# Optimization experiments

Hardware: AMD Instinct MI355X
Metric: run time of the kernel (lower is better)

Reference implementation:

```python
import jax, jax.numpy as jnp
import numpy as np

N = 50000    # nodes
R = 3        # relations
E = 600000   # edges per relation
IN, HID, OUT = 128, 64, 64


def setup_inputs() -> dict:
    key = jax.random.key(0)
    k = jax.random.split(key, 5)
    x = jax.random.normal(k[0], (N, IN), dtype=jnp.float32)
    src = jax.random.randint(k[1], (R, E), 0, N, dtype=jnp.int32)
    dst = jax.random.randint(k[2], (R, E), 0, N, dtype=jnp.int32)
    # glorot-ish init like dgl.nn.GraphConv weight; bias init zeros
    W1 = jax.random.normal(k[3], (R, IN, HID), dtype=jnp.float32) * (IN ** -0.5)
    b1 = jnp.zeros((R, HID), dtype=jnp.float32)
    W2 = jax.random.normal(k[4], (R, HID, OUT), dtype=jnp.float32) * (HID ** -0.5)
    b2 = jnp.zeros((R, OUT), dtype=jnp.float32)
    return {"x": x, "W1": W1, "b1": b1, "W2": W2, "b2": b2, "src": src, "dst": dst}


def _graph_conv(x, src, dst, W, b):
    """dgl.nn.GraphConv with norm='both', single relation.
    x: [N, Fin]; src/dst: [E] int; W: [Fin, Fout]; b: [Fout].
    """
    n = x.shape[0]
    ones = jnp.ones(src.shape[0], dtype=x.dtype)
    out_deg = jax.ops.segment_sum(ones, src, num_segments=n)
    h = x * (jnp.maximum(out_deg, 1.0) ** -0.5)[:, None]   # src-side norm
    if W.shape[0] > W.shape[1]:
        # mult W first, then aggregate (fewer flops per edge)
        h = h @ W
        agg = jax.ops.segment_sum(h[src], dst, num_segments=n)  # [N, Fout]
    else:
        agg = jax.ops.segment_sum(h[src], dst, num_segments=n) @ W
    in_deg = jax.ops.segment_sum(ones, dst, num_segments=n)
    return agg * (jnp.maximum(in_deg, 1.0) ** -0.5)[:, None] + b


def _hetero_conv(x, src, dst, W, b):
    # HeteroGraphConv(aggregate='sum'): run each relation's GraphConv, sum results.
    per_rel = jax.vmap(_graph_conv, in_axes=(None, 0, 0, 0, 0))(x, src, dst, W, b)
    return per_rel.sum(axis=0)  # [N, Fout]


def reference(x, W1, b1, W2, b2, src, dst):
    h = jax.nn.relu(_hetero_conv(x, src, dst, W1, b1))
    return _hetero_conv(h, src, dst, W2, b2)
```

## Files before the change

kernel.cpp:

```cpp
#include <hip/hip_runtime.h>

#define NODES 50000
#define RELS  3
#define NEDGE 600000
#define FIN   128
#define FHID  64
#define FOUT  64
#define SEGS  (RELS * NODES)
#define NBLK  ((SEGS + 255) / 256)

#define HC     96
#define HCHUNK (NEDGE / HC)
#define HBYTES NODES
#define HWORDS (HBYTES / 4)

#define BS     250
#define NBUK   200
#define NBUKT  (RELS * NBUK)
#define CAPLOG 12
#define CAP    (1 << CAPLOG)
#define BCH    192
#define BCHUNK (NEDGE / BCH)

typedef _Float16 half8 __attribute__((ext_vector_type(8)));
typedef float   floatx4 __attribute__((ext_vector_type(4)));

__global__ __launch_bounds__(256) void init_kernel(int* __restrict__ bcur,
                                                   const float* __restrict__ W1,
                                                   const float* __restrict__ W2,
                                                   _Float16* __restrict__ W1t,
                                                   _Float16* __restrict__ W2t) {
    int gid = blockIdx.x * 256 + threadIdx.x;
    if (gid < NBUKT) bcur[gid] = 0;
    int g2 = gid - 1024;
    if (g2 >= 0 && g2 < RELS * FIN * FHID) {
        int r = g2 / (FIN * FHID);
        int rem = g2 - r * FIN * FHID;
        int k = rem / FHID, j = rem - k * FHID;
        W1t[((size_t)r * FHID + j) * FIN + k] = (_Float16)W1[g2];
        return;
    }
    int g3 = g2 - RELS * FIN * FHID;
    if (g3 >= 0 && g3 < RELS * FHID * FOUT) {
        int r = g3 / (FHID * FOUT);
        int rem = g3 - r * FHID * FOUT;
        int k = rem / FOUT, j = rem - k * FOUT;
        W2t[((size_t)r * FOUT + j) * FHID + k] = (_Float16)W2[g3];
    }
}

__global__ __launch_bounds__(1024) void hist_kernel(const int* __restrict__ src,
                                                    unsigned int* __restrict__ slab32) {
    __shared__ unsigned int bins[HWORDS];
    int chunk = blockIdx.x, r = blockIdx.y;
    const int* arr = src + (size_t)r * NEDGE + (size_t)chunk * HCHUNK;
    for (int w = threadIdx.x; w < HWORDS; w += 1024) bins[w] = 0u;
    __syncthreads();
    for (int i = threadIdx.x; i < HCHUNK; i += 1024) {
        int v = arr[i];
        atomicAdd(&bins[v >> 2], 1u << ((v & 3) * 8));
    }
    __syncthreads();
    unsigned int* out = slab32 + ((size_t)(r * HC + chunk)) * HWORDS;
    for (int w = threadIdx.x; w < HWORDS; w += 1024) out[w] = bins[w];
}

__global__ __launch_bounds__(512) void bucketize_kernel(const int* __restrict__ src,
                                                        const int* __restrict__ dst,
                                                        int* __restrict__ bcur,
                                                        unsigned int* __restrict__ rec) {
    __shared__ unsigned int stage[BCHUNK];
    __shared__ int bh[NBUK], bbase[NBUK], blc[NBUK];
    int chunk = blockIdx.x, r = blockIdx.y;
    for (int i = threadIdx.x; i < NBUK; i += 512) { bh[i] = 0; blc[i] = 0; }
    __syncthreads();
    size_t ebase = (size_t)r * NEDGE + (size_t)chunk * BCHUNK;
    for (int i = threadIdx.x; i < BCHUNK; i += 512) {
        int d = dst[ebase + i], s = src[ebase + i];
        int b = d / BS;
        int dl = d - b * BS;
        stage[i] = ((unsigned)s << 16) | ((unsigned)b << 8) | (unsigned)dl;
        atomicAdd(&bh[b], 1);
    }
    __syncthreads();
    for (int i = threadIdx.x; i < NBUK; i += 512)
        bbase[i] = atomicAdd(&bcur[r * NBUK + i], bh[i]);
    __syncthreads();
    for (int i = threadIdx.x; i < BCHUNK; i += 512) {
        unsigned u = stage[i];
        int b = (u >> 8) & 255;
        int slot = bbase[b] + atomicAdd(&blc[b], 1);
        rec[(((size_t)r * NBUK + b) << CAPLOG) + slot] = u;
    }
}

__global__ __launch_bounds__(256) void degbkt_kernel(const unsigned int* __restrict__ rec,
                                                     const int* __restrict__ bcur,
                                                     const unsigned char* __restrict__ slab8,
                                                     int* __restrict__ idI,
                                                     float* __restrict__ innorm,
                                                     float* __restrict__ outnorm) {
    __shared__ int cnt[BS];
    int b = blockIdx.x, r = blockIdx.y;
    for (int i = threadIdx.x; i < BS; i += 256) cnt[i] = 0;
    __syncthreads();
    int n = bcur[r * NBUK + b];
    const unsigned int* rb = rec + (((size_t)r * NBUK + b) << CAPLOG);
    for (int i = threadIdx.x; i < n; i += 256) atomicAdd(&cnt[rb[i] & 255], 1);
    __syncthreads();
    int segbase = r * NODES + b * BS;
    const unsigned char* sl = slab8 + (size_t)r * HC * HBYTES + b * BS;
    for (int i = threadIdx.x; i < BS; i += 256) {
        int c = cnt[i];
        idI[segbase + i] = c;
        innorm[segbase + i] = rsqrtf(fmaxf((float)c, 1.0f));
        int od = 0;
#pragma unroll 4
        for (int ch = 0; ch < HC; ++ch) od += sl[(size_t)ch * HBYTES + i];
        outnorm[segbase + i] = rsqrtf(fmaxf((float)od, 1.0f));
    }
}

__global__ __launch_bounds__(256) void scan_sums_kernel(const int* __restrict__ idI,
                                                        int* __restrict__ partials) {
    __shared__ int s[256];
    int i = blockIdx.x * 256 + threadIdx.x;
    s[threadIdx.x] = (i < SEGS) ? idI[i] : 0;
    __syncthreads();
    for (int off = 128; off > 0; off >>= 1) {
        if (threadIdx.x < off) s[threadIdx.x] += s[threadIdx.x + off];
        __syncthreads();
    }
    if (threadIdx.x == 0) partials[blockIdx.x] = s[0];
}

__global__ __launch_bounds__(256) void scan_write_kernel(const int* __restrict__ idI,
                                                         const int* __restrict__ partials,
                                                         int* __restrict__ offs) {
    __shared__ int sp[1024];
    __shared__ int s[256];
    int tid = threadIdx.x;
    for (int i = tid; i < 1024; i += 256) sp[i] = (i < NBLK) ? partials[i] : 0;
    __syncthreads();
    for (int off = 1; off < 1024; off <<= 1) {
        int v[4];
#pragma unroll
        for (int k = 0; k < 4; ++k) { int i = tid + k * 256; v[k] = (i >= off) ? sp[i - off] : 0; }
        __syncthreads();
#pragma unroll
        for (int k = 0; k < 4; ++k) sp[tid + k * 256] += v[k];
        __syncthreads();
    }
    int bpre = (blockIdx.x == 0) ? 0 : sp[blockIdx.x - 1];
    int i = blockIdx.x * 256 + tid;
    int v = (i < SEGS) ? idI[i] : 0;
    s[tid] = v;
    __syncthreads();
    for (int off = 1; off < 256; off <<= 1) {
        int t = s[tid];
        int add = (tid >= off) ? s[tid - off] : 0;
        __syncthreads();
        s[tid] = t + add;
        __syncthreads();
    }
    if (i < SEGS) offs[i] = bpre + (s[tid] - v);
}

__global__ __launch_bounds__(512) void fillbkt_kernel(const unsigned int* __restrict__ rec,
                                                      const int* __restrict__ bcur,
                                                      const int* __restrict__ offs,
                                                      unsigned short* __restrict__ edge_src) {
    __shared__ int obase[BS];
    __shared__ int lcur[BS];
    int b = blockIdx.x, r = blockIdx.y;
    int segbase = r * NODES + b * BS;
    for (int i = threadIdx.x; i < BS; i += 512) {
        obase[i] = offs[segbase + i];
        lcur[i] = 0;
    }
    __syncthreads();
    int n = bcur[r * NBUK + b];
    const unsigned int* rb = rec + (((size_t)r * NBUK + b) << CAPLOG);
    for (int i = threadIdx.x; i < n; i += 512) {
        unsigned u = rb[i];
        int dl = u & 255;
        int pos = obase[dl] + atomicAdd(&lcur[dl], 1);
        edge_src[pos] = (unsigned short)(u >> 16);
    }
}

__global__ __launch_bounds__(256, 4) void gemm1_kernel(const float* __restrict__ x,
                                                       const _Float16* __restrict__ W1t,
                                                       const float* __restrict__ outnorm,
                                                       _Float16* __restrict__ h) {
    int lane = threadIdx.x & 63;
    int wv   = threadIdx.x >> 6;
    int m = lane & 15, quad = lane >> 4;
    int n0 = (blockIdx.x * 4 + wv) * 16;
    if (n0 + 16 > NODES) n0 = NODES - 16;
    const float* xrow = x + (size_t)(n0 + m) * FIN + quad * 8;

    floatx4 acc[12];
#pragma unroll
    for (int t = 0; t < 12; ++t) acc[t] = (floatx4){0.f, 0.f, 0.f, 0.f};

#pragma unroll 1
    for (int ks = 0; ks < 4; ++ks) {
        float4 xa = *(const float4*)(xrow + ks * 32);
        float4 xb = *(const float4*)(xrow + ks * 32 + 4);
        half8 a;
        a[0] = (_Float16)xa.x; a[1] = (_Float16)xa.y;
        a[2] = (_Float16)xa.z; a[3] = (_Float16)xa.w;
        a[4] = (_Float16)xb.x; a[5] = (_Float16)xb.y;
        a[6] = (_Float16)xb.z; a[7] = (_Float16)xb.w;
#pragma unroll
        for (int jt = 0; jt < 12; ++jt) {
            const _Float16* bp = W1t + ((size_t)jt * 16 + m) * FIN + ks * 32 + quad * 8;
            half8 b = *(const half8*)bp;
            acc[jt] = __builtin_amdgcn_mfma_f32_16x16x32_f16(a, b, acc[jt], 0, 0, 0);
        }
    }

#pragma unroll
    for (int jt = 0; jt < 12; ++jt) {
        int r = jt >> 2;
        int j = (jt & 3) * 16 + m;
        _Float16* hb = h + (size_t)r * NODES * FHID;
        const float* on = outnorm + r * NODES;
#pragma unroll
        for (int reg = 0; reg < 4; ++reg) {
            int node = n0 + quad * 4 + reg;
            hb[(size_t)node * FHID + j] = (_Float16)(acc[jt][reg] * on[node]);
        }
    }
}

__device__ __forceinline__ void seg_sum8(const _Float16* __restrict__ hb,
                                         const unsigned short* __restrict__ es,
                                         int o, int c, int q, float* __restrict__ s) {
#pragma unroll
    for (int i = 0; i < 8; ++i) s[i] = 0.f;
    int t = 0;
    for (; t + 4 <= c; t += 4) {
        int i0 = es[o + t], i1 = es[o + t + 1], i2 = es[o + t + 2], i3 = es[o + t + 3];
        half8 v0 = *(const half8*)(hb + (size_t)i0 * FHID + q * 8);
        half8 v1 = *(const half8*)(hb + (size_t)i1 * FHID + q * 8);
        half8 v2 = *(const half8*)(hb + (size_t)i2 * FHID + q * 8);
        half8 v3 = *(const half8*)(hb + (size_t)i3 * FHID + q * 8);
#pragma unroll
        for (int i = 0; i < 8; ++i) {
            s[i] += (float)v0[i];
            s[i] += (float)v1[i];
            s[i] += (float)v2[i];
            s[i] += (float)v3[i];
        }
    }
    if (t + 2 <= c) {
        int i0 = es[o + t], i1 = es[o + t + 1];
        half8 v0 = *(const half8*)(hb + (size_t)i0 * FHID + q * 8);
        half8 v1 = *(const half8*)(hb + (size_t)i1 * FHID + q * 8);
#pragma unroll
        for (int i = 0; i < 8; ++i) {
            s[i] += (float)v0[i];
            s[i] += (float)v1[i];
        }
        t += 2;
    }
    if (t < c) {
        int i0 = es[o + t];
        half8 v0 = *(const half8*)(hb + (size_t)i0 * FHID + q * 8);
#pragma unroll
        for (int i = 0; i < 8; ++i) s[i] += (float)v0[i];
    }
}

__global__ __launch_bounds__(256) void gather1_kernel(const _Float16* __restrict__ h,
                                                      const unsigned short* __restrict__ es,
                                                      const int* __restrict__ offs,
                                                      const int* __restrict__ cnt,
                                                      const float* __restrict__ innorm,
                                                      const float* __restrict__ b1,
                                                      _Float16* __restrict__ B) {
    int lane = threadIdx.x & 63;
    int wv   = threadIdx.x >> 6;
    int w    = blockIdx.x * 4 + wv;
    if (w * 8 >= NODES) return;
    int q    = lane & 7;
    int e8   = lane >> 3;
    int d    = w * 8 + e8;
    int c0 = cnt[d], c1 = cnt[NODES + d], c2 = cnt[2 * NODES + d];
    int o0 = offs[d], o1 = offs[NODES + d], o2 = offs[2 * NODES + d];
    float w0 = innorm[d], w1 = innorm[NODES + d], w2 = innorm[2 * NODES + d];

    float tot[8], s[8];
    seg_sum8(h, es, o0, c0, q, s);
#pragma unroll
    for (int i = 0; i < 8; ++i) tot[i] = w0 * s[i];
    seg_sum8(h + (size_t)NODES * FHID, es, o1, c1, q, s);
#pragma unroll
    for (int i = 0; i < 8; ++i) tot[i] = fmaf(w1, s[i], tot[i]);
    seg_sum8(h + 2 * (size_t)NODES * FHID, es, o2, c2, q, s);
#pragma unroll
    for (int i = 0; i < 8; ++i) tot[i] = fmaf(w2, s[i], tot[i]);

    half8 o8;
#pragma unroll
    for (int i = 0; i < 8; ++i) {
        int j = q * 8 + i;
        float bs = b1[j] + b1[FHID + j] + b1[2 * FHID + j];
        o8[i] = (_Float16)fmaxf(tot[i] + bs, 0.f);
    }
    *(half8*)(B + (size_t)d * FHID + q * 8) = o8;
}

__global__ __launch_bounds__(256) void gather2_kernel(const _Float16* __restrict__ h1,
                                                      const unsigned short* __restrict__ es,
                                                      const int* __restrict__ offs,
                                                      const int* __restrict__ cnt,
                                                      const float* __restrict__ outnorm,
                                                      const float* __restrict__ innorm,
                                                      _Float16* __restrict__ A2) {
    int lane = threadIdx.x & 63;
    int wv   = threadIdx.x >> 6;
    int w    = blockIdx.x * 4 + wv;
    int s0   = w * 8;
    if (s0 >= SEGS) return;
    int q    = lane & 7;
    int e8   = lane >> 3;
    int seg  = s0 + e8;
    int o = offs[seg], c = cnt[seg];
    const float* on = outnorm + (s0 / NODES) * NODES;

    float tot[8];
#pragma unroll
    for (int i = 0; i < 8; ++i) tot[i] = 0.f;
    int t = 0;
    for (; t + 4 <= c; t += 4) {
        int i0 = es[o + t], i1 = es[o + t + 1], i2 = es[o + t + 2], i3 = es[o + t + 3];
        float w0 = on[i0], w1 = on[i1], w2 = on[i2], w3 = on[i3];
        half8 v0 = *(const half8*)(h1 + (size_t)i0 * FHID + q * 8);
        half8 v1 = *(const half8*)(h1 + (size_t)i1 * FHID + q * 8);
        half8 v2 = *(const half8*)(h1 + (size_t)i2 * FHID + q * 8);
        half8 v3 = *(const half8*)(h1 + (size_t)i3 * FHID + q * 8);
#pragma unroll
        for (int i = 0; i < 8; ++i) {
            tot[i] = fmaf(w0, (float)v0[i], tot[i]);
            tot[i] = fmaf(w1, (float)v1[i], tot[i]);
            tot[i] = fmaf(w2, (float)v2[i], tot[i]);
            tot[i] = fmaf(w3, (float)v3[i], tot[i]);
        }
    }
    if (t + 2 <= c) {
        int i0 = es[o + t], i1 = es[o + t + 1];
        float w0 = on[i0], w1 = on[i1];
        half8 v0 = *(const half8*)(h1 + (size_t)i0 * FHID + q * 8);
        half8 v1 = *(const half8*)(h1 + (size_t)i1 * FHID + q * 8);
#pragma unroll
        for (int i = 0; i < 8; ++i) {
            tot[i] = fmaf(w0, (float)v0[i], tot[i]);
            tot[i] = fmaf(w1, (float)v1[i], tot[i]);
        }
        t += 2;
    }
    if (t < c) {
        int i0 = es[o + t];
        float w0 = on[i0];
        half8 v0 = *(const half8*)(h1 + (size_t)i0 * FHID + q * 8);
#pragma unroll
        for (int i = 0; i < 8; ++i) tot[i] = fmaf(w0, (float)v0[i], tot[i]);
    }

    float inr = innorm[seg];
    half8 o8;
#pragma unroll
    for (int i = 0; i < 8; ++i) o8[i] = (_Float16)(inr * tot[i]);
    *(half8*)(A2 + (size_t)seg * FHID + q * 8) = o8;
}

__global__ __launch_bounds__(256, 4) void out_kernel(const _Float16* __restrict__ A2,
                                                     const _Float16* __restrict__ W2t,
                                                     const float* __restrict__ b2,
                                                     float* __restrict__ out) {
    int lane = threadIdx.x & 63;
    int wv   = threadIdx.x >> 6;
    int m = lane & 15, quad = lane >> 4;
    int n0 = (blockIdx.x * 4 + wv) * 16;
    if (n0 + 16 > NODES) n0 = NODES - 16;

    floatx4 acc[4];
#pragma unroll
    for (int t = 0; t < 4; ++t) acc[t] = (floatx4){0.f, 0.f, 0.f, 0.f};

#pragma unroll 1
    for (int kk = 0; kk < 6; ++kk) {
        int r = kk >> 1, kb = (kk & 1) * 32;
        const _Float16* ap = A2 + ((size_t)r * NODES + n0 + m) * FHID + kb + quad * 8;
        half8 a = *(const half8*)ap;
#pragma unroll
        for (int jt = 0; jt < 4; ++jt) {
            const _Float16* bp = W2t + ((size_t)(r * FOUT + jt * 16 + m)) * FHID + kb + quad * 8;
            half8 b = *(const half8*)bp;
            acc[jt] = __builtin_amdgcn_mfma_f32_16x16x32_f16(a, b, acc[jt], 0, 0, 0);
        }
    }

#pragma unroll
    for (int jt = 0; jt < 4; ++jt) {
        int j = jt * 16 + m;
        float bs = b2[j] + b2[FOUT + j] + b2[2 * FOUT + j];
#pragma unroll
        for (int reg = 0; reg < 4; ++reg) {
            int node = n0 + quad * 4 + reg;
            out[(size_t)node * FOUT + j] = acc[jt][reg] + bs;
        }
    }
}

extern "C" void kernel_launch(void* const* d_in, const int* in_sizes, int n_in,
                              void* d_out, int out_size, void* d_ws, size_t ws_size,
                              hipStream_t stream) {
    const float* x   = (const float*)d_in[0];
    const float* W1  = (const float*)d_in[1];
    const float* b1  = (const float*)d_in[2];
    const float* W2  = (const float*)d_in[3];
    const float* b2  = (const float*)d_in[4];
    const int*   src = (const int*)d_in[5];
    const int*   dst = (const int*)d_in[6];
    float* out = (float*)d_out;

    int*   idI      = (int*)d_ws;
    int*   offs     = idI + SEGS;
    int*   partials = offs + SEGS;
    int*   bcur     = partials + 1024;
    unsigned short* edge_src = (unsigned short*)(bcur + 1024);
    float* outnorm  = (float*)(edge_src + (size_t)RELS * NEDGE);
    float* innorm   = outnorm + SEGS;
    _Float16* W1t   = (_Float16*)(innorm + SEGS);
    _Float16* W2t   = W1t + (size_t)RELS * FHID * FIN;
    _Float16* h     = W2t + (size_t)RELS * FHID * FOUT;
    _Float16* B     = h + (size_t)SEGS * FHID;
    _Float16* A2    = B + (size_t)NODES * FHID;
    unsigned int*  rec    = (unsigned int*)h;
    unsigned int*  slab32 = rec + (size_t)NBUKT * CAP;
    unsigned char* slab8  = (unsigned char*)slab32;

    const int GW = ((NODES / 16) + 4) / 4;

    init_kernel<<<(1024 + RELS * FIN * FHID + RELS * FHID * FOUT + 255) / 256,
                  256, 0, stream>>>(bcur, W1, W2, W1t, W2t);
    hist_kernel<<<dim3(HC, RELS), 1024, 0, stream>>>(src, slab32);
    bucketize_kernel<<<dim3(BCH, RELS), 512, 0, stream>>>(src, dst, bcur, rec);
    degbkt_kernel<<<dim3(NBUK, RELS), 256, 0, stream>>>(rec, bcur, slab8, idI, innorm, outnorm);
    scan_sums_kernel<<<NBLK, 256, 0, stream>>>(idI, partials);
    scan_write_kernel<<<NBLK, 256, 0, stream>>>(idI, partials, offs);
    fillbkt_kernel<<<dim3(NBUK, RELS), 512, 0, stream>>>(rec, bcur, offs, edge_src);

    gemm1_kernel<<<GW, 256, 0, stream>>>(x, W1t, outnorm, h);
    gather1_kernel<<<(NODES / 8 + 3) / 4, 256, 0, stream>>>(h, edge_src, offs, idI, innorm, b1, B);

    gather2_kernel<<<(SEGS / 8 + 3) / 4, 256, 0, stream>>>(B, edge_src, offs, idI, outnorm, innorm, A2);
    out_kernel<<<GW, 256, 0, stream>>>(A2, W2t, b2, out);
}
```

Baseline: 250.0 us.

## Fuse preprocessing kernels and compute offsets from bucket counts; deepen gather unroll

Folds the init work (bcur reset, weight transpose/convert) into the histogram kernel. It merges degree counting, the two-pass prefix scan and edge filling into one kernel, which derives each bucket's global offset by summing earlier bucket counts. The gather loops now issue eight row loads at a time instead of four. The aim is to cut kernel launches and scan passes and to raise memory-level parallelism in the gathers, at the cost of each degfill block redundantly summing up to 600 bucket counts and higher register use in the gathers.

New measurement: 238.5 us. -4.6%, faster.

```diff
diff --git a/kernel.cpp b/kernel.cpp
--- a/kernel.cpp
+++ b/kernel.cpp
@@ -7,7 +7,6 @@
 #define FHID  64
 #define FOUT  64
 #define SEGS  (RELS * NODES)
-#define NBLK  ((SEGS + 255) / 256)
 
 #define HC     96
 #define HCHUNK (NEDGE / HC)
@@ -25,32 +24,13 @@
 typedef _Float16 half8 __attribute__((ext_vector_type(8)));
 typedef float   floatx4 __attribute__((ext_vector_type(4)));
 
-__global__ __launch_bounds__(256) void init_kernel(int* __restrict__ bcur,
-                                                   const float* __restrict__ W1,
-                                                   const float* __restrict__ W2,
-                                                   _Float16* __restrict__ W1t,
-                                                   _Float16* __restrict__ W2t) {
-    int gid = blockIdx.x * 256 + threadIdx.x;
-    if (gid < NBUKT) bcur[gid] = 0;
-    int g2 = gid - 1024;
-    if (g2 >= 0 && g2 < RELS * FIN * FHID) {
-        int r = g2 / (FIN * FHID);
-        int rem = g2 - r * FIN * FHID;
-        int k = rem / FHID, j = rem - k * FHID;
-        W1t[((size_t)r * FHID + j) * FIN + k] = (_Float16)W1[g2];
-        return;
-    }
-    int g3 = g2 - RELS * FIN * FHID;
-    if (g3 >= 0 && g3 < RELS * FHID * FOUT) {
-        int r = g3 / (FHID * FOUT);
-        int rem = g3 - r * FHID * FOUT;
-        int k = rem / FOUT, j = rem - k * FOUT;
-        W2t[((size_t)r * FOUT + j) * FHID + k] = (_Float16)W2[g3];
-    }
-}
-
 __global__ __launch_bounds__(1024) void hist_kernel(const int* __restrict__ src,
-                                                    unsigned int* __restrict__ slab32) {
+                                                    unsigned int* __restrict__ slab32,
+                                                    int* __restrict__ bcur,
+                                                    const float* __restrict__ W1,
+                                                    const float* __restrict__ W2,
+                                                    _Float16* __restrict__ W1t,
+                                                    _Float16* __restrict__ W2t) {
     __shared__ unsigned int bins[HWORDS];
     int chunk = blockIdx.x, r = blockIdx.y;
     const int* arr = src + (size_t)r * NEDGE + (size_t)chunk * HCHUNK;
@@ -63,6 +43,26 @@
     __syncthreads();
     unsigned int* out = slab32 + ((size_t)(r * HC + chunk)) * HWORDS;
     for (int w = threadIdx.x; w < HWORDS; w += 1024) out[w] = bins[w];
+
+    if (r == 0) {
+        int gid = chunk * 1024 + threadIdx.x;
+        if (gid < NBUKT) bcur[gid] = 0;
+        int g2 = gid - 1024;
+        if (g2 >= 0 && g2 < RELS * FIN * FHID) {
+            int rr = g2 / (FIN * FHID);
+            int rem = g2 - rr * FIN * FHID;
+            int k = rem / FHID, j = rem - k * FHID;
+            W1t[((size_t)rr * FHID + j) * FIN + k] = (_Float16)W1[g2];
+            return;
+        }
+        int g3 = g2 - RELS * FIN * FHID;
+        if (g3 >= 0 && g3 < RELS * FHID * FOUT) {
+            int rr = g3 / (FHID * FOUT);
+            int rem = g3 - rr * FHID * FOUT;
+            int k = rem / FOUT, j = rem - k * FOUT;
+            W2t[((size_t)rr * FOUT + j) * FHID + k] = (_Float16)W2[g3];
+        }
+    }
 }
 
 __global__ __launch_bounds__(512) void bucketize_kernel(const int* __restrict__ src,
@@ -94,94 +94,58 @@
     }
 }
 
-__global__ __launch_bounds__(256) void degbkt_kernel(const unsigned int* __restrict__ rec,
-                                                     const int* __restrict__ bcur,
-                                                     const unsigned char* __restrict__ slab8,
-                                                     int* __restrict__ idI,
-                                                     float* __restrict__ innorm,
-                                                     float* __restrict__ outnorm) {
-    __shared__ int cnt[BS];
+__global__ __launch_bounds__(512) void degfill_kernel(const unsigned int* __restrict__ rec,
+                                                      const int* __restrict__ bcur,
+                                                      const unsigned char* __restrict__ slab8,
+                                                      int* __restrict__ idI,
+                                                      float* __restrict__ innorm,
+                                                      float* __restrict__ outnorm,
+                                                      int* __restrict__ offs,
+                                                      unsigned short* __restrict__ edge_src) {
+    __shared__ int cnt[BS], lcur[BS], obase[BS];
+    __shared__ int red[512];
+    int tid = threadIdx.x;
     int b = blockIdx.x, r = blockIdx.y;
-    for (int i = threadIdx.x; i < BS; i += 256) cnt[i] = 0;
-    __syncthreads();
-    int n = bcur[r * NBUK + b];
-    const unsigned int* rb = rec + (((size_t)r * NBUK + b) << CAPLOG);
-    for (int i = threadIdx.x; i < n; i += 256) atomicAdd(&cnt[rb[i] & 255], 1);
-    __syncthreads();
+    int gbid = r * NBUK + b;
+    for (int i = tid; i < BS; i += 512) { cnt[i] = 0; lcur[i] = 0; }
+    __syncthreads();
+    int n = bcur[gbid];
+    const unsigned int* rb = rec + ((size_t)gbid << CAPLOG);
+    for (int i = tid; i < n; i += 512) atomicAdd(&cnt[rb[i] & 255], 1);
+    int p = 0;
+    for (int i = tid; i < gbid; i += 512) p += bcur[i];
+    red[tid] = p;
+    __syncthreads();
+    for (int off = 256; off > 0; off >>= 1) {
+        if (tid < off) red[tid] += red[tid + off];
+        __syncthreads();
+    }
+    int bpre = red[0];
+    int v = (tid < BS) ? cnt[tid] : 0;
+    __syncthreads();
+    red[tid] = v;
+    __syncthreads();
+    for (int off = 1; off < 512; off <<= 1) {
+        int add = (tid >= off) ? red[tid - off] : 0;
+        __syncthreads();
+        red[tid] += add;
+        __syncthreads();
+    }
     int segbase = r * NODES + b * BS;
-    const unsigned char* sl = slab8 + (size_t)r * HC * HBYTES + b * BS;
-    for (int i = threadIdx.x; i < BS; i += 256) {
-        int c = cnt[i];
-        idI[segbase + i] = c;
-        innorm[segbase + i] = rsqrtf(fmaxf((float)c, 1.0f));
+    if (tid < BS) {
+        int o = bpre + (red[tid] - v);
+        obase[tid] = o;
+        offs[segbase + tid] = o;
+        idI[segbase + tid] = v;
+        innorm[segbase + tid] = rsqrtf(fmaxf((float)v, 1.0f));
         int od = 0;
+        const unsigned char* sl = slab8 + (size_t)r * HC * HBYTES + b * BS;
 #pragma unroll 4
-        for (int ch = 0; ch < HC; ++ch) od += sl[(size_t)ch * HBYTES + i];
-        outnorm[segbase + i] = rsqrtf(fmaxf((float)od, 1.0f));
-    }
-}
-
-__global__ __launch_bounds__(256) void scan_sums_kernel(const int* __restrict__ idI,
-                                                        int* __restrict__ partials) {
-    __shared__ int s[256];
-    int i = blockIdx.x * 256 + threadIdx.x;
-    s[threadIdx.x] = (i < SEGS) ? idI[i] : 0;
-    __syncthreads();
-    for (int off = 128; off > 0; off >>= 1) {
-        if (threadIdx.x < off) s[threadIdx.x] += s[threadIdx.x + off];
-        __syncthreads();
-    }
-    if (threadIdx.x == 0) partials[blockIdx.x] = s[0];
-}
-
-__global__ __launch_bounds__(256) void scan_write_kernel(const int* __restrict__ idI,
-                                                         const int* __restrict__ partials,
-                                                         int* __restrict__ offs) {
-    __shared__ int sp[1024];
-    __shared__ int s[256];
-    int tid = threadIdx.x;
-    for (int i = tid; i < 1024; i += 256) sp[i] = (i < NBLK) ? partials[i] : 0;
-    __syncthreads();
-    for (int off = 1; off < 1024; off <<= 1) {
-        int v[4];
-#pragma unroll
-        for (int k = 0; k < 4; ++k) { int i = tid + k * 256; v[k] = (i >= off) ? sp[i - off] : 0; }
-        __syncthreads();
-#pragma unroll
-        for (int k = 0; k < 4; ++k) sp[tid + k * 256] += v[k];
-        __syncthreads();
-    }
-    int bpre = (blockIdx.x == 0) ? 0 : sp[blockIdx.x - 1];
-    int i = blockIdx.x * 256 + tid;
-    int v = (i < SEGS) ? idI[i] : 0;
-    s[tid] = v;
-    __syncthreads();
-    for (int off = 1; off < 256; off <<= 1) {
-        int t = s[tid];
-        int add = (tid >= off) ? s[tid - off] : 0;
-        __syncthreads();
-        s[tid] = t + add;
-        __syncthreads();
-    }
-    if (i < SEGS) offs[i] = bpre + (s[tid] - v);
-}
-
-__global__ __launch_bounds__(512) void fillbkt_kernel(const unsigned int* __restrict__ rec,
-                                                      const int* __restrict__ bcur,
-                                                      const int* __restrict__ offs,
-                                                      unsigned short* __restrict__ edge_src) {
-    __shared__ int obase[BS];
-    __shared__ int lcur[BS];
-    int b = blockIdx.x, r = blockIdx.y;
-    int segbase = r * NODES + b * BS;
-    for (int i = threadIdx.x; i < BS; i += 512) {
-        obase[i] = offs[segbase + i];
-        lcur[i] = 0;
-    }
-    __syncthreads();
-    int n = bcur[r * NBUK + b];
-    const unsigned int* rb = rec + (((size_t)r * NBUK + b) << CAPLOG);
-    for (int i = threadIdx.x; i < n; i += 512) {
+        for (int ch = 0; ch < HC; ++ch) od += sl[(size_t)ch * HBYTES + tid];
+        outnorm[segbase + tid] = rsqrtf(fmaxf((float)od, 1.0f));
+    }
+    __syncthreads();
+    for (int i = tid; i < n; i += 512) {
         unsigned u = rb[i];
         int dl = u & 255;
         int pos = obase[dl] + atomicAdd(&lcur[dl], 1);
@@ -241,19 +205,30 @@
 #pragma unroll
     for (int i = 0; i < 8; ++i) s[i] = 0.f;
     int t = 0;
-    for (; t + 4 <= c; t += 4) {
-        int i0 = es[o + t], i1 = es[o + t + 1], i2 = es[o + t + 2], i3 = es[o + t + 3];
-        half8 v0 = *(const half8*)(hb + (size_t)i0 * FHID + q * 8);
-        half8 v1 = *(const half8*)(hb + (size_t)i1 * FHID + q * 8);
-        half8 v2 = *(const half8*)(hb + (size_t)i2 * FHID + q * 8);
-        half8 v3 = *(const half8*)(hb + (size_t)i3 * FHID + q * 8);
-#pragma unroll
-        for (int i = 0; i < 8; ++i) {
-            s[i] += (float)v0[i];
-            s[i] += (float)v1[i];
-            s[i] += (float)v2[i];
-            s[i] += (float)v3[i];
-        }
+    for (; t + 8 <= c; t += 8) {
+        int ix[8];
+        half8 v[8];
+#pragma unroll
+        for (int k = 0; k < 8; ++k) ix[k] = es[o + t + k];
+#pragma unroll
+        for (int k = 0; k < 8; ++k) v[k] = *(const half8*)(hb + (size_t)ix[k] * FHID + q * 8);
+#pragma unroll
+        for (int k = 0; k < 8; ++k)
+#pragma unroll
+            for (int i = 0; i < 8; ++i) s[i] += (float)v[k][i];
+    }
+    if (t + 4 <= c) {
+        int ix[4];
+        half8 v[4];
+#pragma unroll
+        for (int k = 0; k < 4; ++k) ix[k] = es[o + t + k];
+#pragma unroll
+        for (int k = 0; k < 4; ++k) v[k] = *(const half8*)(hb + (size_t)ix[k] * FHID + q * 8);
+#pragma unroll
+        for (int k = 0; k < 4; ++k)
+#pragma unroll
+            for (int i = 0; i < 8; ++i) s[i] += (float)v[k][i];
+        t += 4;
     }
     if (t + 2 <= c) {
         int i0 = es[o + t], i1 = es[o + t + 1];
@@ -335,20 +310,36 @@
 #pragma unroll
     for (int i = 0; i < 8; ++i) tot[i] = 0.f;
     int t = 0;
-    for (; t + 4 <= c; t += 4) {
-        int i0 = es[o + t], i1 = es[o + t + 1], i2 = es[o + t + 2], i3 = es[o + t + 3];
-        float w0 = on[i0], w1 = on[i1], w2 = on[i2], w3 = on[i3];
-        half8 v0 = *(const half8*)(h1 + (size_t)i0 * FHID + q * 8);
-        half8 v1 = *(const half8*)(h1 + (size_t)i1 * FHID + q * 8);
-        half8 v2 = *(const half8*)(h1 + (size_t)i2 * FHID + q * 8);
-        half8 v3 = *(const half8*)(h1 + (size_t)i3 * FHID + q * 8);
-#pragma unroll
-        for (int i = 0; i < 8; ++i) {
-            tot[i] = fmaf(w0, (float)v0[i], tot[i]);
-            tot[i] = fmaf(w1, (float)v1[i], tot[i]);
-            tot[i] = fmaf(w2, (float)v2[i], tot[i]);
-            tot[i] = fmaf(w3, (float)v3[i], tot[i]);
-        }
+    for (; t + 8 <= c; t += 8) {
+        int ix[8];
+        float wk[8];
+        half8 v[8];
+#pragma unroll
+        for (int k = 0; k < 8; ++k) ix[k] = es[o + t + k];
+#pragma unroll
+        for (int k = 0; k < 8; ++k) wk[k] = on[ix[k]];
+#pragma unroll
+        for (int k = 0; k < 8; ++k) v[k] = *(const half8*)(h1 + (size_t)ix[k] * FHID + q * 8);
+#pragma unroll
+        for (int k = 0; k < 8; ++k)
+#pragma unroll
+            for (int i = 0; i < 8; ++i) tot[i] = fmaf(wk[k], (float)v[k][i], tot[i]);
+    }
+    if (t + 4 <= c) {
+        int ix[4];
+        float wk[4];
+        half8 v[4];
+#pragma unroll
+        for (int k = 0; k < 4; ++k) ix[k] = es[o + t + k];
+#pragma unroll
+        for (int k = 0; k < 4; ++k) wk[k] = on[ix[k]];
+#pragma unroll
+        for (int k = 0; k < 4; ++k) v[k] = *(const half8*)(h1 + (size_t)ix[k] * FHID + q * 8);
+#pragma unroll
+        for (int k = 0; k < 4; ++k)
+#pragma unroll
+            for (int i = 0; i < 8; ++i) tot[i] = fmaf(wk[k], (float)v[k][i], tot[i]);
+        t += 4;
     }
     if (t + 2 <= c) {
         int i0 = es[o + t], i1 = es[o + t + 1];
@@ -430,8 +421,7 @@
 
     int*   idI      = (int*)d_ws;
     int*   offs     = idI + SEGS;
-    int*   partials = offs + SEGS;
-    int*   bcur     = partials + 1024;
+    int*   bcur     = offs + SEGS;
     unsigned short* edge_src = (unsigned short*)(bcur + 1024);
     float* outnorm  = (float*)(edge_src + (size_t)RELS * NEDGE);
     float* innorm   = outnorm + SEGS;
@@ -446,14 +436,10 @@
 
     const int GW = ((NODES / 16) + 4) / 4;
 
-    init_kernel<<<(1024 + RELS * FIN * FHID + RELS * FHID * FOUT + 255) / 256,
-                  256, 0, stream>>>(bcur, W1, W2, W1t, W2t);
-    hist_kernel<<<dim3(HC, RELS), 1024, 0, stream>>>(src, slab32);
+    hist_kernel<<<dim3(HC, RELS), 1024, 0, stream>>>(src, slab32, bcur, W1, W2, W1t, W2t);
     bucketize_kernel<<<dim3(BCH, RELS), 512, 0, stream>>>(src, dst, bcur, rec);
-    degbkt_kernel<<<dim3(NBUK, RELS), 256, 0, stream>>>(rec, bcur, slab8, idI, innorm, outnorm);
-    scan_sums_kernel<<<NBLK, 256, 0, stream>>>(idI, partials);
-    scan_write_kernel<<<NBLK, 256, 0, stream>>>(idI, partials, offs);
-    fillbkt_kernel<<<dim3(NBUK, RELS), 512, 0, stream>>>(rec, bcur, offs, edge_src);
+    degfill_kernel<<<dim3(NBUK, RELS), 512, 0, stream>>>(rec, bcur, slab8, idI, innorm,
+                                                         outnorm, offs, edge_src);
 
     gemm1_kernel<<<GW, 256, 0, stream>>>(x, W1t, outnorm, h);
     gather1_kernel<<<(NODES / 8 + 3) / 4, 256, 0, stream>>>(h, edge_src, offs, idI, innorm, b1, B);
```
